# Kernel optimization log

Hardware: AMD Instinct MI355X
Metric: run time of the kernel (lower is better)

The kernel has to match this reference:

```python
import jax, jax.numpy as jnp
import numpy as np

B, HH, WW, C, HEADS = 8, 56, 56, 384, 6
DIM_OUT = 384


def _upsample2x_bilinear(x):
    # x: [..., m, n] -> [..., 2m, 2n]; matches torch F.interpolate bilinear align_corners=False
    m, n = x.shape[-2], x.shape[-1]
    def coords(inn):
        c = (jnp.arange(2 * inn) + 0.5) / 2.0 - 0.5
        c = jnp.clip(c, 0.0, inn - 1)
        i0 = jnp.floor(c).astype(jnp.int32)
        i1 = jnp.minimum(i0 + 1, inn - 1)
        return i0, i1, (c - i0).astype(x.dtype)
    i0, i1, wy = coords(m)
    j0, j1, wx = coords(n)
    rows = x[..., i0, :] * (1 - wy)[:, None] + x[..., i1, :] * wy[:, None]
    return rows[..., :, j0] * (1 - wx) + rows[..., :, j1] * wx


def setup_inputs() -> dict:
    key = jax.random.key(0)
    ks = jax.random.split(key, 12)
    inp = {
        'x': jax.random.normal(ks[0], (B, HH * WW, C), jnp.float32),
        'res_attn': jax.random.normal(ks[1], (B, HEADS, (HH // 4) * (WW // 4), (HH // 2) * (WW // 2)), jnp.float32),
        'conv_q_w': jax.random.normal(ks[2], (C, 1, 3, 3), jnp.float32) * 0.05,
        'ln_g': jnp.ones((C,), jnp.float32),
        'ln_b': jnp.zeros((C,), jnp.float32),
        'wq': jax.random.normal(ks[3], (DIM_OUT, C), jnp.float32) * 0.02,
        'wk': jax.random.normal(ks[4], (DIM_OUT, C), jnp.float32) * 0.02,
        'wv': jax.random.normal(ks[5], (DIM_OUT, C), jnp.float32) * 0.02,
        'w_proj': jax.random.normal(ks[6], (DIM_OUT, DIM_OUT), jnp.float32) * 0.02,
        'b_proj': jnp.zeros((DIM_OUT,), jnp.float32),
        'w_fuse': jax.random.normal(ks[7], (HEADS, 2 * HEADS, 1, 1), jnp.float32) * 0.1,
        'b_fuse': jnp.zeros((HEADS,), jnp.float32),
        'h': HH,
        'w': WW,
    }
    return inp


def reference(x, res_attn, conv_q_w, ln_g, ln_b, wq, wk, wv, w_proj, b_proj, w_fuse, b_fuse, h, w):
    Bz, _, Cc = x.shape
    heads = w_fuse.shape[0]
    xi = x.transpose(0, 2, 1).reshape(Bz, Cc, h, w)  # b c h w
    # conv_proj_q: depthwise conv k3 s2 p1 (no bias), then LayerNorm
    q = jax.lax.conv_general_dilated(
        xi, conv_q_w, (2, 2), ((1, 1), (1, 1)),
        dimension_numbers=('NCHW', 'OIHW', 'NCHW'), feature_group_count=Cc)
    hq, wq2 = q.shape[2], q.shape[3]
    q = q.reshape(Bz, Cc, hq * wq2).transpose(0, 2, 1)  # b t c
    mu = q.mean(-1, keepdims=True)
    var = ((q - mu) ** 2).mean(-1, keepdims=True)
    q = (q - mu) / jnp.sqrt(var + 1e-5) * ln_g + ln_b
    # conv_proj_k/v: avg pool k2 s2 p0
    kv = xi.reshape(Bz, Cc, h // 2, 2, w // 2, 2).mean(axis=(3, 5))
    kv = kv.reshape(Bz, Cc, (h // 2) * (w // 2)).transpose(0, 2, 1)  # b t c
    dim_out = wq.shape[0]
    dh = dim_out // heads
    def split(t):
        return t.reshape(Bz, t.shape[1], heads, dh).transpose(0, 2, 1, 3)
    qh = split(q @ wq.T)
    kh = split(kv @ wk.T)
    vh = split(kv @ wv.T)
    scale = dim_out ** -0.5
    attn_score = jnp.einsum('bhlk,bhtk->bhlt', qh, kh) * scale  # [B,H,L,T]
    sh, sw = h // 4, w // 4
    a = res_attn.shape[-1]
    rx = res_attn[:, :, :sh * sw, :]
    rx = rx.reshape(Bz * heads, sh * sw, a).transpose(0, 2, 1).reshape(Bz * heads, a, sh, sw)
    rx = _upsample2x_bilinear(rx)  # (b h) a 2sh 2sw
    rx = rx.reshape(Bz, heads, a, 4 * sh * sw).transpose(0, 1, 3, 2)  # b h L a
    cat = jnp.concatenate([attn_score, rx], axis=1)  # [B, 2H, L, T]
    attn_score = jnp.einsum('bclt,oc->bolt', cat, w_fuse[:, :, 0, 0]) + b_fuse[None, :, None, None]
    attn = jax.nn.softmax(attn_score, axis=-1)
    out = jnp.einsum('bhlt,bhtv->bhlv', attn, vh)
    out = out.transpose(0, 2, 1, 3).reshape(Bz, -1, dim_out)
    return out @ w_proj.T + b_proj
```

## Files before the change

kernel.cpp:

```cpp
#include <hip/hip_runtime.h>

typedef unsigned int uint;
typedef unsigned short ushort_t;
typedef short bf16x8 __attribute__((ext_vector_type(8)));
typedef float f32x4 __attribute__((ext_vector_type(4)));

__device__ __forceinline__ ushort_t f2bf(float f) {
  uint u = __builtin_bit_cast(uint, f);
  u += 0x7fffu + ((u >> 16) & 1u);
  return (ushort_t)(u >> 16);
}
__device__ __forceinline__ float bf2f(ushort_t s) {
  return __builtin_bit_cast(float, (uint)s << 16);
}
__device__ __forceinline__ bf16x8 ld_frag(const ushort_t* p) {
  return __builtin_bit_cast(bf16x8, *(const uint4*)p);
}

__global__ __launch_bounds__(384) void k_convln(
    const float* __restrict__ x, const float* __restrict__ wc,
    const float* __restrict__ g, const float* __restrict__ bb,
    ushort_t* __restrict__ qout, ushort_t* __restrict__ kvout)
{
  const int b  = blockIdx.x / 784;
  const int t  = blockIdx.x % 784;
  const int oy = t / 28, ox = t % 28;
  const int c  = threadIdx.x;
  const float* xb = x + (size_t)b * 3136 * 384 + c;
  float acc = 0.f, pv = 0.f;
  #pragma unroll
  for (int ky = 0; ky < 3; ky++) {
    const int iy = 2 * oy - 1 + ky;
    const bool yok = (iy >= 0) & (iy < 56);
    #pragma unroll
    for (int kx = 0; kx < 3; kx++) {
      const int ix = 2 * ox - 1 + kx;
      if (yok & (ix >= 0) & (ix < 56)) {
        const float xv = xb[(size_t)(iy * 56 + ix) * 384];
        acc += wc[c * 9 + ky * 3 + kx] * xv;
        if ((ky >= 1) & (kx >= 1)) pv += xv;
      }
    }
  }
  kvout[((size_t)b * 784 + t) * 384 + c] = f2bf(pv * 0.25f);
  float s = acc, s2 = acc * acc;
  #pragma unroll
  for (int off = 32; off >= 1; off >>= 1) {
    s  += __shfl_xor(s,  off);
    s2 += __shfl_xor(s2, off);
  }
  __shared__ float ps[6], ps2[6];
  if ((c & 63) == 0) { ps[c >> 6] = s; ps2[c >> 6] = s2; }
  __syncthreads();
  float S = 0.f, S2 = 0.f;
  #pragma unroll
  for (int i = 0; i < 6; i++) { S += ps[i]; S2 += ps2[i]; }
  const float mu  = S * (1.f / 384.f);
  const float var = S2 * (1.f / 384.f) - mu * mu;
  const float inv = rsqrtf(var + 1e-5f);
  qout[((size_t)b * 784 + t) * 384 + c] = f2bf((acc - mu) * inv * g[c] + bb[c]);
}

__global__ __launch_bounds__(256) void k_wcvt(
    const float* __restrict__ a, const float* __restrict__ b,
    const float* __restrict__ c, const float* __restrict__ d,
    ushort_t* __restrict__ oa, ushort_t* __restrict__ ob,
    ushort_t* __restrict__ oc, ushort_t* __restrict__ od)
{
  const int i = blockIdx.x * 256 + threadIdx.x;
  if (i < 147456) {
    oa[i] = f2bf(a[i]); ob[i] = f2bf(b[i]);
    oc[i] = f2bf(c[i]); od[i] = f2bf(d[i]);
  }
}

__global__ __launch_bounds__(256) void k_gemm3(
    const ushort_t* __restrict__ Xq, const ushort_t* __restrict__ Xkv,
    const ushort_t* __restrict__ Wq, const ushort_t* __restrict__ Wk,
    const ushort_t* __restrict__ Wv,
    ushort_t* __restrict__ Qo, ushort_t* __restrict__ Ko,
    ushort_t* __restrict__ Vo)
{
  __shared__ ushort_t As[128][40];
  __shared__ ushort_t Bs[128][40];
  const int z = blockIdx.z;
  const ushort_t* X = (z == 0) ? Xq : Xkv;
  const ushort_t* W = (z == 0) ? Wq : (z == 1) ? Wk : Wv;
  const int tid = threadIdx.x, w = tid >> 6, lane = tid & 63;
  const int quad = lane >> 4, r = lane & 15;
  const int m0 = blockIdx.y * 128, n0 = blockIdx.x * 128;
  const int wm = w >> 1, wn = w & 1;
  const int lr = tid >> 2, lc = (tid & 3) << 3;
  const ushort_t* xp = X + (size_t)(m0 + lr) * 384 + lc;
  const ushort_t* wp = W + (size_t)(n0 + lr) * 384 + lc;
  f32x4 acc[4][4] = {};
  for (int k0 = 0; k0 < 384; k0 += 32) {
    __syncthreads();
    *(uint4*)&As[lr][lc]      = *(const uint4*)(xp + k0);
    *(uint4*)&As[lr + 64][lc] = *(const uint4*)(xp + (size_t)64 * 384 + k0);
    *(uint4*)&Bs[lr][lc]      = *(const uint4*)(wp + k0);
    *(uint4*)&Bs[lr + 64][lc] = *(const uint4*)(wp + (size_t)64 * 384 + k0);
    __syncthreads();
    bf16x8 af[4], bf_[4];
    #pragma unroll
    for (int mt = 0; mt < 4; mt++) af[mt]  = *(const bf16x8*)&As[wm * 64 + mt * 16 + r][quad * 8];
    #pragma unroll
    for (int nt = 0; nt < 4; nt++) bf_[nt] = *(const bf16x8*)&Bs[wn * 64 + nt * 16 + r][quad * 8];
    #pragma unroll
    for (int mt = 0; mt < 4; mt++)
      #pragma unroll
      for (int nt = 0; nt < 4; nt++)
        acc[mt][nt] = __builtin_amdgcn_mfma_f32_16x16x32_bf16(af[mt], bf_[nt], acc[mt][nt], 0, 0, 0);
  }
  #pragma unroll
  for (int mt = 0; mt < 4; mt++) {
    #pragma unroll
    for (int nt = 0; nt < 4; nt++) {
      #pragma unroll
      for (int i = 0; i < 4; i++) {
        const int row = m0 + wm * 64 + mt * 16 + quad * 4 + i;
        const int col = n0 + wn * 64 + nt * 16 + r;
        const float v = acc[mt][nt][i];
        if (z < 2) {
          ushort_t* Y = (z == 0) ? Qo : Ko;
          Y[(size_t)row * 384 + col] = f2bf(v);
        } else {
          const int bb = row / 784, tt = row % 784;
          Vo[((size_t)bb * 384 + col) * 784 + tt] = f2bf(v);
        }
      }
    }
  }
}

__global__ __launch_bounds__(256) void k_gemmo(
    const ushort_t* __restrict__ X, const ushort_t* __restrict__ W,
    const float* __restrict__ bias, float* __restrict__ Y)
{
  __shared__ ushort_t As[128][40];
  __shared__ ushort_t Bs[128][40];
  const int tid = threadIdx.x, w = tid >> 6, lane = tid & 63;
  const int quad = lane >> 4, r = lane & 15;
  const int m0 = blockIdx.y * 128, n0 = blockIdx.x * 128;
  const int wm = w >> 1, wn = w & 1;
  const int lr = tid >> 2, lc = (tid & 3) << 3;
  const ushort_t* xp = X + (size_t)(m0 + lr) * 384 + lc;
  const ushort_t* wp = W + (size_t)(n0 + lr) * 384 + lc;
  f32x4 acc[4][4] = {};
  for (int k0 = 0; k0 < 384; k0 += 32) {
    __syncthreads();
    *(uint4*)&As[lr][lc]      = *(const uint4*)(xp + k0);
    *(uint4*)&As[lr + 64][lc] = *(const uint4*)(xp + (size_t)64 * 384 + k0);
    *(uint4*)&Bs[lr][lc]      = *(const uint4*)(wp + k0);
    *(uint4*)&Bs[lr + 64][lc] = *(const uint4*)(wp + (size_t)64 * 384 + k0);
    __syncthreads();
    bf16x8 af[4], bf_[4];
    #pragma unroll
    for (int mt = 0; mt < 4; mt++) af[mt]  = *(const bf16x8*)&As[wm * 64 + mt * 16 + r][quad * 8];
    #pragma unroll
    for (int nt = 0; nt < 4; nt++) bf_[nt] = *(const bf16x8*)&Bs[wn * 64 + nt * 16 + r][quad * 8];
    #pragma unroll
    for (int mt = 0; mt < 4; mt++)
      #pragma unroll
      for (int nt = 0; nt < 4; nt++)
        acc[mt][nt] = __builtin_amdgcn_mfma_f32_16x16x32_bf16(af[mt], bf_[nt], acc[mt][nt], 0, 0, 0);
  }
  #pragma unroll
  for (int mt = 0; mt < 4; mt++) {
    #pragma unroll
    for (int nt = 0; nt < 4; nt++) {
      #pragma unroll
      for (int i = 0; i < 4; i++) {
        const int row = m0 + wm * 64 + mt * 16 + quad * 4 + i;
        const int col = n0 + wn * 64 + nt * 16 + r;
        Y[(size_t)row * 384 + col] = acc[mt][nt][i] + bias[col];
      }
    }
  }
}

__global__ __launch_bounds__(256) void k_qkfuse(
    const ushort_t* __restrict__ Qb, const ushort_t* __restrict__ Kb,
    const float* __restrict__ ra, const float* __restrict__ w_fuse,
    const float* __restrict__ b_fuse, ushort_t* __restrict__ P)
{
  const int tid = threadIdx.x, w = tid >> 6, lane = tid & 63;
  const int quad = lane >> 4, r = lane & 15;
  const int b  = blockIdx.z;
  const int m0 = blockIdx.y * 64 + w * 16;
  const int t0 = blockIdx.x * 32;

  __shared__ float wf[72], bfu[6];
  if (tid < 72) wf[tid] = w_fuse[tid] * ((tid % 12) < 6 ? 0.05103103630798288f : 1.f);
  if (tid < 6)  bfu[tid] = b_fuse[tid];
  __syncthreads();

  const int lq = min(m0 + r, 783);
  const ushort_t* qp = Qb + (size_t)(b * 784 + lq) * 384 + quad * 8;
  bf16x8 qf[6][2];
  #pragma unroll
  for (int h = 0; h < 6; h++) {
    qf[h][0] = ld_frag(qp + h * 64);
    qf[h][1] = ld_frag(qp + h * 64 + 32);
  }
  f32x4 acc[6][2] = {};
  #pragma unroll
  for (int j = 0; j < 2; j++) {
    const int t = min(t0 + j * 16 + r, 783);
    const ushort_t* kp = Kb + (size_t)(b * 784 + t) * 384 + quad * 8;
    #pragma unroll
    for (int h = 0; h < 6; h++) {
      acc[h][j] = __builtin_amdgcn_mfma_f32_16x16x32_bf16(
          qf[h][0], ld_frag(kp + h * 64),      acc[h][j], 0, 0, 0);
      acc[h][j] = __builtin_amdgcn_mfma_f32_16x16x32_bf16(
          qf[h][1], ld_frag(kp + h * 64 + 32), acc[h][j], 0, 0, 0);
    }
  }

  int p00a[4], p01a[4], p10a[4], p11a[4];
  float w00a[4], w01a[4], w10a[4], w11a[4];
  #pragma unroll
  for (int i = 0; i < 4; i++) {
    const int l = min(m0 + quad * 4 + i, 783);
    const int Y = l / 28, X = l % 28;
    const float cy = fminf(fmaxf((float)Y * 0.5f - 0.25f, 0.f), 13.f);
    const float cx = fminf(fmaxf((float)X * 0.5f - 0.25f, 0.f), 13.f);
    const int y0 = (int)cy, y1 = min(y0 + 1, 13);
    const int x0 = (int)cx, x1 = min(x0 + 1, 13);
    const float fy = cy - (float)y0, fx = cx - (float)x0;
    w00a[i] = (1.f - fy) * (1.f - fx); w01a[i] = (1.f - fy) * fx;
    w10a[i] = fy * (1.f - fx);         w11a[i] = fy * fx;
    p00a[i] = (y0 * 14 + x0) * 784; p01a[i] = (y0 * 14 + x1) * 784;
    p10a[i] = (y1 * 14 + x0) * 784; p11a[i] = (y1 * 14 + x1) * 784;
  }
  const float* rab = ra + (size_t)b * 6 * 153664;

  #pragma unroll
  for (int j = 0; j < 2; j++) {
    const int t = t0 + j * 16 + r;
    if (t < 784) {
      #pragma unroll
      for (int i = 0; i < 4; i++) {
        const int lo = m0 + quad * 4 + i;
        if (lo < 784) {
          float a[6];
          #pragma unroll
          for (int o = 0; o < 6; o++) a[o] = bfu[o];
          #pragma unroll
          for (int c = 0; c < 6; c++) {
            const float* rc = rab + (size_t)c * 153664;
            const float rx = w00a[i] * rc[p00a[i] + t] + w01a[i] * rc[p01a[i] + t]
                           + w10a[i] * rc[p10a[i] + t] + w11a[i] * rc[p11a[i] + t];
            const float sv = acc[c][j][i];
            #pragma unroll
            for (int o = 0; o < 6; o++)
              a[o] += wf[o * 12 + c] * sv + wf[o * 12 + 6 + c] * rx;
          }
          ushort_t* prow = P + ((size_t)(b * 784 + lo) * 6) * 784 + t;
          #pragma unroll
          for (int o = 0; o < 6; o++)
            prow[(size_t)o * 784] = f2bf(__expf(fminf(a[o], 60.f)));
        }
      }
    }
  }
}

__global__ __launch_bounds__(256) void k_pvs(
    const ushort_t* __restrict__ P, const ushort_t* __restrict__ Vt,
    ushort_t* __restrict__ O)
{
  const int tid = threadIdx.x, w = tid >> 6, lane = tid & 63;
  const int quad = lane >> 4, r = lane & 15;
  const int bo = blockIdx.y, b = bo / 6, o = bo % 6;
  const int m0 = blockIdx.x * 64 + w * 16;
  const int lq = min(m0 + r, 783);
  const ushort_t* ap = P + ((size_t)(b * 784 + lq) * 6 + o) * 784 + quad * 8;
  const ushort_t* bp = Vt + ((size_t)b * 384 + o * 64 + r) * 784 + quad * 8;
  f32x4 acc[4] = {};
  float ps = 0.f;
  for (int kk = 0; kk < 25; kk++) {
    const int k0 = kk * 32;
    const bool full = (kk < 24) | (quad < 2);
    bf16x8 af = {}, bf_[4] = {};
    if (full) {
      af = ld_frag(ap + k0);
      const ushort_t* sv = (const ushort_t*)&af;
      #pragma unroll
      for (int e = 0; e < 8; e++) ps += bf2f(sv[e]);
      #pragma unroll
      for (int nt = 0; nt < 4; nt++) bf_[nt] = ld_frag(bp + (size_t)nt * 16 * 784 + k0);
    }
    #pragma unroll
    for (int nt = 0; nt < 4; nt++)
      acc[nt] = __builtin_amdgcn_mfma_f32_16x16x32_bf16(af, bf_[nt], acc[nt], 0, 0, 0);
  }
  ps += __shfl_xor(ps, 16);
  ps += __shfl_xor(ps, 32);
  float inv[4];
  #pragma unroll
  for (int i = 0; i < 4; i++) inv[i] = 1.f / __shfl(ps, quad * 4 + i);
  #pragma unroll
  for (int nt = 0; nt < 4; nt++) {
    #pragma unroll
    for (int i = 0; i < 4; i++) {
      const int lo = m0 + quad * 4 + i;
      if (lo < 784)
        O[(size_t)(b * 784 + lo) * 384 + o * 64 + nt * 16 + r] =
            f2bf(acc[nt][i] * inv[i]);
    }
  }
}

extern "C" void kernel_launch(void* const* d_in, const int* in_sizes, int n_in,
                              void* d_out, int out_size, void* d_ws, size_t ws_size,
                              hipStream_t stream)
{
  const float* x        = (const float*)d_in[0];
  const float* res_attn = (const float*)d_in[1];
  const float* conv_w   = (const float*)d_in[2];
  const float* ln_g     = (const float*)d_in[3];
  const float* ln_b     = (const float*)d_in[4];
  const float* wq       = (const float*)d_in[5];
  const float* wk       = (const float*)d_in[6];
  const float* wv       = (const float*)d_in[7];
  const float* w_proj   = (const float*)d_in[8];
  const float* b_proj   = (const float*)d_in[9];
  const float* w_fuse   = (const float*)d_in[10];
  const float* b_fuse   = (const float*)d_in[11];
  float* out = (float*)d_out;

  const size_t NE = (size_t)8 * 784 * 384;
  const size_t NW = 147456;
  ushort_t* q_ln_b = (ushort_t*)d_ws;
  ushort_t* kv_b   = q_ln_b + NE;
  ushort_t* Qb     = kv_b + NE;
  ushort_t* Kb     = Qb + NE;
  ushort_t* Vt     = Kb + NE;
  ushort_t* Opre   = Vt + NE;
  ushort_t* wqb    = Opre + NE;
  ushort_t* wkb    = wqb + NW;
  ushort_t* wvb    = wkb + NW;
  ushort_t* wpb    = wvb + NW;
  ushort_t* P      = wpb + NW;

  k_convln<<<dim3(8 * 784), dim3(384), 0, stream>>>(x, conv_w, ln_g, ln_b, q_ln_b, kv_b);
  k_wcvt  <<<dim3(576),     dim3(256), 0, stream>>>(wq, wk, wv, w_proj, wqb, wkb, wvb, wpb);

  k_gemm3<<<dim3(3, 49, 3), dim3(256), 0, stream>>>(
      q_ln_b, kv_b, wqb, wkb, wvb, Qb, Kb, Vt);

  k_qkfuse<<<dim3(25, 13, 8), dim3(256), 0, stream>>>(
      Qb, Kb, res_attn, w_fuse, b_fuse, P);
  k_pvs<<<dim3(13, 48), dim3(256), 0, stream>>>(P, Vt, Opre);

  k_gemmo<<<dim3(3, 49), dim3(256), 0, stream>>>(Opre, wpb, b_proj, out);
}
```

Measured before the change: 339.6 us.

## Split fused QK-score/residual-fuse kernel into a per-head QK GEMM and a coalesced fuse pass

Replaces the single kernel that computed QK scores for all heads and immediately mixed them with the upsampled residual attention. A per-(batch, head) MFMA kernel now writes bf16 scores into the P buffer. A separate per-row kernel then reads those scores and the res_attn taps with fully contiguous t-indexed accesses, applies the 1x1 head fusion and exp, and writes the result in place. The aim is to get coalesced res_attn reads and simpler register use. The cost is an extra full write and read of the bf16 score tensor, plus an extra bf16 rounding of raw scores before the fuse.

```diff
diff --git a/kernel.cpp b/kernel.cpp
--- a/kernel.cpp
+++ b/kernel.cpp
@@ -179,89 +179,81 @@
   }
 }
 
-__global__ __launch_bounds__(256) void k_qkfuse(
+__global__ __launch_bounds__(256) void k_qk(
     const ushort_t* __restrict__ Qb, const ushort_t* __restrict__ Kb,
-    const float* __restrict__ ra, const float* __restrict__ w_fuse,
-    const float* __restrict__ b_fuse, ushort_t* __restrict__ P)
+    ushort_t* __restrict__ S)
 {
   const int tid = threadIdx.x, w = tid >> 6, lane = tid & 63;
   const int quad = lane >> 4, r = lane & 15;
-  const int b  = blockIdx.z;
+  const int bh = blockIdx.z, b = bh / 6, h = bh % 6;
   const int m0 = blockIdx.y * 64 + w * 16;
-  const int t0 = blockIdx.x * 32;
-
+  const int t0 = blockIdx.x * 112;
+  const int lq = min(m0 + r, 783);
+  const ushort_t* qp = Qb + (size_t)(b * 784 + lq) * 384 + h * 64 + quad * 8;
+  const bf16x8 a0 = ld_frag(qp), a1 = ld_frag(qp + 32);
+  f32x4 acc[7] = {};
+  #pragma unroll
+  for (int j = 0; j < 7; j++) {
+    const int t = t0 + j * 16 + r;
+    const ushort_t* kp = Kb + (size_t)(b * 784 + t) * 384 + h * 64 + quad * 8;
+    acc[j] = __builtin_amdgcn_mfma_f32_16x16x32_bf16(a0, ld_frag(kp),      acc[j], 0, 0, 0);
+    acc[j] = __builtin_amdgcn_mfma_f32_16x16x32_bf16(a1, ld_frag(kp + 32), acc[j], 0, 0, 0);
+  }
+  #pragma unroll
+  for (int j = 0; j < 7; j++) {
+    #pragma unroll
+    for (int i = 0; i < 4; i++) {
+      const int lo = m0 + quad * 4 + i;
+      if (lo < 784)
+        S[((size_t)(b * 784 + lo) * 6 + h) * 784 + t0 + j * 16 + r] = f2bf(acc[j][i]);
+    }
+  }
+}
+
+__global__ __launch_bounds__(256) void k_fusex(
+    ushort_t* __restrict__ S, const float* __restrict__ ra,
+    const float* __restrict__ w_fuse, const float* __restrict__ b_fuse)
+{
+  const int tid = threadIdx.x;
+  const int bl = blockIdx.x, b = bl / 784, l = bl % 784;
   __shared__ float wf[72], bfu[6];
   if (tid < 72) wf[tid] = w_fuse[tid] * ((tid % 12) < 6 ? 0.05103103630798288f : 1.f);
   if (tid < 6)  bfu[tid] = b_fuse[tid];
   __syncthreads();
 
-  const int lq = min(m0 + r, 783);
-  const ushort_t* qp = Qb + (size_t)(b * 784 + lq) * 384 + quad * 8;
-  bf16x8 qf[6][2];
-  #pragma unroll
-  for (int h = 0; h < 6; h++) {
-    qf[h][0] = ld_frag(qp + h * 64);
-    qf[h][1] = ld_frag(qp + h * 64 + 32);
-  }
-  f32x4 acc[6][2] = {};
-  #pragma unroll
-  for (int j = 0; j < 2; j++) {
-    const int t = min(t0 + j * 16 + r, 783);
-    const ushort_t* kp = Kb + (size_t)(b * 784 + t) * 384 + quad * 8;
-    #pragma unroll
-    for (int h = 0; h < 6; h++) {
-      acc[h][j] = __builtin_amdgcn_mfma_f32_16x16x32_bf16(
-          qf[h][0], ld_frag(kp + h * 64),      acc[h][j], 0, 0, 0);
-      acc[h][j] = __builtin_amdgcn_mfma_f32_16x16x32_bf16(
-          qf[h][1], ld_frag(kp + h * 64 + 32), acc[h][j], 0, 0, 0);
-    }
-  }
-
-  int p00a[4], p01a[4], p10a[4], p11a[4];
-  float w00a[4], w01a[4], w10a[4], w11a[4];
-  #pragma unroll
-  for (int i = 0; i < 4; i++) {
-    const int l = min(m0 + quad * 4 + i, 783);
-    const int Y = l / 28, X = l % 28;
-    const float cy = fminf(fmaxf((float)Y * 0.5f - 0.25f, 0.f), 13.f);
-    const float cx = fminf(fmaxf((float)X * 0.5f - 0.25f, 0.f), 13.f);
-    const int y0 = (int)cy, y1 = min(y0 + 1, 13);
-    const int x0 = (int)cx, x1 = min(x0 + 1, 13);
-    const float fy = cy - (float)y0, fx = cx - (float)x0;
-    w00a[i] = (1.f - fy) * (1.f - fx); w01a[i] = (1.f - fy) * fx;
-    w10a[i] = fy * (1.f - fx);         w11a[i] = fy * fx;
-    p00a[i] = (y0 * 14 + x0) * 784; p01a[i] = (y0 * 14 + x1) * 784;
-    p10a[i] = (y1 * 14 + x0) * 784; p11a[i] = (y1 * 14 + x1) * 784;
-  }
-  const float* rab = ra + (size_t)b * 6 * 153664;
-
-  #pragma unroll
-  for (int j = 0; j < 2; j++) {
-    const int t = t0 + j * 16 + r;
+  const int Y = l / 28, X = l % 28;
+  const float cy = fminf(fmaxf((float)Y * 0.5f - 0.25f, 0.f), 13.f);
+  const float cx = fminf(fmaxf((float)X * 0.5f - 0.25f, 0.f), 13.f);
+  const int y0 = (int)cy, y1 = min(y0 + 1, 13);
+  const int x0 = (int)cx, x1 = min(x0 + 1, 13);
+  const float fy = cy - (float)y0, fx = cx - (float)x0;
+  const float w00 = (1.f - fy) * (1.f - fx), w01 = (1.f - fy) * fx;
+  const float w10 = fy * (1.f - fx),         w11 = fy * fx;
+  const int p00 = (y0 * 14 + x0) * 784, p01 = (y0 * 14 + x1) * 784;
+  const int p10 = (y1 * 14 + x0) * 784, p11 = (y1 * 14 + x1) * 784;
+
+  ushort_t* Srow = S + (size_t)bl * 6 * 784;
+  const float* rab = ra + (size_t)b * 6 * 196 * 784;
+
+  #pragma unroll
+  for (int j = 0; j < 4; j++) {
+    const int t = tid + j * 256;
     if (t < 784) {
-      #pragma unroll
-      for (int i = 0; i < 4; i++) {
-        const int lo = m0 + quad * 4 + i;
-        if (lo < 784) {
-          float a[6];
-          #pragma unroll
-          for (int o = 0; o < 6; o++) a[o] = bfu[o];
-          #pragma unroll
-          for (int c = 0; c < 6; c++) {
-            const float* rc = rab + (size_t)c * 153664;
-            const float rx = w00a[i] * rc[p00a[i] + t] + w01a[i] * rc[p01a[i] + t]
-                           + w10a[i] * rc[p10a[i] + t] + w11a[i] * rc[p11a[i] + t];
-            const float sv = acc[c][j][i];
-            #pragma unroll
-            for (int o = 0; o < 6; o++)
-              a[o] += wf[o * 12 + c] * sv + wf[o * 12 + 6 + c] * rx;
-          }
-          ushort_t* prow = P + ((size_t)(b * 784 + lo) * 6) * 784 + t;
-          #pragma unroll
-          for (int o = 0; o < 6; o++)
-            prow[(size_t)o * 784] = f2bf(__expf(fminf(a[o], 60.f)));
-        }
+      float a[6];
+      #pragma unroll
+      for (int o = 0; o < 6; o++) a[o] = bfu[o];
+      #pragma unroll
+      for (int c = 0; c < 6; c++) {
+        const float* rc = rab + (size_t)c * (196 * 784);
+        const float rx = w00 * rc[p00 + t] + w01 * rc[p01 + t]
+                       + w10 * rc[p10 + t] + w11 * rc[p11 + t];
+        const float sv = bf2f(Srow[c * 784 + t]);
+        #pragma unroll
+        for (int o = 0; o < 6; o++) a[o] += wf[o * 12 + c] * sv + wf[o * 12 + 6 + c] * rx;
       }
+      #pragma unroll
+      for (int o = 0; o < 6; o++)
+        Srow[o * 784 + t] = f2bf(__expf(fminf(a[o], 60.f)));
     }
   }
 }
@@ -342,7 +334,7 @@
   ushort_t* wkb    = wqb + NW;
   ushort_t* wvb    = wkb + NW;
   ushort_t* wpb    = wvb + NW;
-  ushort_t* P      = wpb + NW;
+  ushort_t* S      = wpb + NW;
 
   k_convln<<<dim3(8 * 784), dim3(384), 0, stream>>>(x, conv_w, ln_g, ln_b, q_ln_b, kv_b);
   k_wcvt  <<<dim3(576),     dim3(256), 0, stream>>>(wq, wk, wv, w_proj, wqb, wkb, wvb, wpb);
@@ -350,9 +342,9 @@
   k_gemm3<<<dim3(3, 49, 3), dim3(256), 0, stream>>>(
       q_ln_b, kv_b, wqb, wkb, wvb, Qb, Kb, Vt);
 
-  k_qkfuse<<<dim3(25, 13, 8), dim3(256), 0, stream>>>(
-      Qb, Kb, res_attn, w_fuse, b_fuse, P);
-  k_pvs<<<dim3(13, 48), dim3(256), 0, stream>>>(P, Vt, Opre);
+  k_qk   <<<dim3(7, 13, 48), dim3(256), 0, stream>>>(Qb, Kb, S);
+  k_fusex<<<dim3(8 * 784),   dim3(256), 0, stream>>>(S, res_attn, w_fuse, b_fuse);
+  k_pvs  <<<dim3(13, 48),    dim3(256), 0, stream>>>(S, Vt, Opre);
 
   k_gemmo<<<dim3(3, 49), dim3(256), 0, stream>>>(Opre, wpb, b_proj, out);
 }
```

Result: faster. 306.9 us (-9.6%).
